# Kernel optimization log

Measured on AMD Instinct MI355X. Metric: run time of the kernel, lower is better.

Reference implementation:

```python
import jax, jax.numpy as jnp
import numpy as np

B, C, H, W, K = 4, 96, 56, 56, 9
CM = 2 * C  # graph-conv output channels (standard Grapher: 2*in_channels)


def setup_inputs() -> dict:
    key = jax.random.key(0)
    ks = jax.random.split(key, 6)
    x = jax.random.normal(ks[0], (B, C, H, W), jnp.float32)
    fc1_w = jax.random.normal(ks[1], (C, C), jnp.float32) * 0.05
    fc1_b = jnp.zeros((C,), jnp.float32)
    gconv_w = jax.random.normal(ks[2], (CM, 2 * C), jnp.float32) * 0.05
    gconv_b = jnp.zeros((CM,), jnp.float32)
    fc2_w = jax.random.normal(ks[3], (C, CM), jnp.float32) * 0.05
    fc2_b = jnp.zeros((C,), jnp.float32)
    sa_w = jax.random.normal(ks[4], (1, 2, 7, 7), jnp.float32) * 0.05
    return dict(x=x, fc1_w=fc1_w, fc1_b=fc1_b, gconv_w=gconv_w, gconv_b=gconv_b,
                fc2_w=fc2_w, fc2_b=fc2_b, sa_w=sa_w)


def _knn_idx(xf, k):
    # xf: (B, C, N) -> (B, N, k) nearest-neighbor indices (includes self),
    # matching dense_knn_matrix: topk of negative squared euclidean distance.
    x2 = jnp.sum(xf * xf, axis=1)                       # (B, N)
    inner = jnp.einsum('bcn,bcm->bnm', xf, xf)          # (B, N, N)
    dist = x2[:, :, None] - 2.0 * inner + x2[:, None, :]
    _, idx = jax.lax.top_k(-dist, k)                    # (B, N, k)
    return idx


def _grapher(x, fc1_w, fc1_b, gconv_w, gconv_b, fc2_w, fc2_b, sa_w):
    shortcut = x
    # fc1: 1x1 conv C -> C
    h = jnp.einsum('bchw,oc->bohw', x, fc1_w) + fc1_b[None, :, None, None]
    b, c, hh, ww = h.shape
    n = hh * ww
    xf = h.reshape(b, c, n)                              # nodes: (B, C, N)
    idx = _knn_idx(xf, K)                                # dynamic KNN graph
    # EdgeConv2d: gather x_j at neighbor indices, x_i = center
    xt = jnp.transpose(xf, (0, 2, 1))                    # (B, N, C)
    x_j = jax.vmap(lambda t, i: t[i])(xt, idx)           # (B, N, K, C)
    x_j = jnp.transpose(x_j, (0, 3, 1, 2))               # (B, C, N, K)
    x_i = xf[:, :, :, None]                              # (B, C, N, 1)
    feat = jnp.concatenate(
        [jnp.broadcast_to(x_i, x_j.shape), x_j - x_i], axis=1)  # (B, 2C, N, K)
    e = jnp.einsum('bcnk,oc->bonk', feat, gconv_w) + gconv_b[None, :, None, None]
    e = jax.nn.relu(e)
    g = jnp.max(e, axis=-1)                              # max over K neighbors
    g = g.reshape(b, CM, hh, ww)
    # fc2: 1x1 conv 2C -> C
    out = jnp.einsum('bchw,oc->bohw', g, fc2_w) + fc2_b[None, :, None, None]
    # SpatialAttention: channel mean/max -> 7x7 conv -> sigmoid gate
    avg = jnp.mean(out, axis=1, keepdims=True)
    mx = jnp.max(out, axis=1, keepdims=True)
    sa_in = jnp.concatenate([avg, mx], axis=1)           # (B, 2, H, W)
    att = jax.lax.conv_general_dilated(
        sa_in, sa_w, window_strides=(1, 1), padding=[(3, 3), (3, 3)],
        dimension_numbers=('NCHW', 'OIHW', 'NCHW'))
    att = jax.nn.sigmoid(att)
    return out * att + shortcut


def reference(x, fc1_w, fc1_b, gconv_w, gconv_b, fc2_w, fc2_b, sa_w):
    return _grapher(x, fc1_w, fc1_b, gconv_w, gconv_b, fc2_w, fc2_b, sa_w)
```

## Files before the change

### kernel.cpp

```cpp
#include <hip/hip_runtime.h>

#define BB 4
#define CC 96
#define NN 3136
#define FLTMAX 3.402823466e+38f
#define CAP 44
#define DELTA 1.0f
#define PREF_MARGIN 0.8f

typedef unsigned short ushort_t;
typedef __attribute__((ext_vector_type(8))) short bf16x8;
typedef __attribute__((ext_vector_type(4))) float f32x4;

__device__ __forceinline__ ushort_t f2bf(float f) {
    unsigned u = __float_as_uint(f);
    unsigned r = (u + 0x7fff + ((u >> 16) & 1)) >> 16;
    return (ushort_t)r;
}
__device__ __forceinline__ float bf2f(ushort_t us) {
    return __uint_as_float(((unsigned)us) << 16);
}


__global__ __launch_bounds__(256) void k_fc1(const float* __restrict__ x, const float* __restrict__ w,
                                             const float* __restrict__ bias, float* __restrict__ h,
                                             float* __restrict__ x2g,
                                             ushort_t* __restrict__ hAhi,
                                             float* __restrict__ hT) {
    __shared__ float sm[96 * 98 + 96 * 64];
    float* wT = sm;
    float* xl = sm + 96 * 98;
    const int tid = threadIdx.x;
    const int n0 = blockIdx.x * 64;
    const int b = blockIdx.y;
    for (int i = tid; i < 96 * 96; i += 256) {
        int o = i / 96, c = i - o * 96;
        wT[c * 98 + o] = w[i];
    }
    const float* xb = x + (size_t)b * CC * NN;
    for (int i = tid; i < 96 * 64; i += 256) {
        int c = i >> 6, nl = i & 63;
        xl[i] = xb[(size_t)c * NN + n0 + nl];
    }
    __syncthreads();
    const int tr = tid >> 4, tc = tid & 15;
    float acc[6][4];
#pragma unroll
    for (int i = 0; i < 6; ++i)
#pragma unroll
        for (int j = 0; j < 4; ++j) acc[i][j] = 0.f;
#pragma unroll 4
    for (int c = 0; c < 96; ++c) {
        float4 xv = *(const float4*)&xl[c * 64 + tc * 4];
        const float* wp = &wT[c * 98 + tr * 6];
        float2 w01 = *(const float2*)(wp);
        float2 w23 = *(const float2*)(wp + 2);
        float2 w45 = *(const float2*)(wp + 4);
        float wv[6] = {w01.x, w01.y, w23.x, w23.y, w45.x, w45.y};
        float xj[4] = {xv.x, xv.y, xv.z, xv.w};
#pragma unroll
        for (int i = 0; i < 6; ++i)
#pragma unroll
            for (int j = 0; j < 4; ++j) acc[i][j] = fmaf(wv[i], xj[j], acc[i][j]);
    }
    float* hb = h + (size_t)b * CC * NN;
    float* hTb = hT + (size_t)b * NN * 96;
    ushort_t* thi = hAhi + (size_t)b * 602112;
#pragma unroll
    for (int i = 0; i < 6; ++i) {
        float bi = bias[tr * 6 + i];
        acc[i][0] += bi; acc[i][1] += bi; acc[i][2] += bi; acc[i][3] += bi;
        float4 o4 = make_float4(acc[i][0], acc[i][1], acc[i][2], acc[i][3]);
        *(float4*)&hb[(size_t)(tr * 6 + i) * NN + n0 + tc * 4] = o4;
        const int c = tr * 6 + i;
        const int cpart = c >> 3;
#pragma unroll
        for (int j = 0; j < 4; ++j) {
            const int n = n0 + tc * 4 + j;
            const int idx = (((n >> 5) * 12 + cpart) * 32 + (n & 31)) * 8 + (c & 7);
            thi[idx] = f2bf(acc[i][j]);
            hTb[(size_t)n * 96 + c] = acc[i][j];
        }
    }
    __syncthreads();
#pragma unroll
    for (int j = 0; j < 4; ++j) {
        float s = 0.f;
#pragma unroll
        for (int i = 0; i < 6; ++i) s = fmaf(acc[i][j], acc[i][j], s);
        sm[tr * 64 + tc * 4 + j] = s;
    }
    __syncthreads();
    if (tid < 64) {
        float s = 0.f;
#pragma unroll
        for (int t = 0; t < 16; ++t) s += sm[t * 64 + tid];
        x2g[(size_t)b * NN + n0 + tid] = s;
    }
}

#define MFMA_TILE_HI(t, acc0, acc1, acc2, acc3)                                       \
    {                                                                                 \
        const int abase_ = (t) * 6144;                                                \
        _Pragma("unroll")                                                             \
        for (int ks_ = 0; ks_ < 3; ++ks_) {                                           \
            const int base_ = abase_ + ks_ * 1024;                                    \
            bf16x8 a0_ = *(const bf16x8*)(hHi + base_ + aoff0);                       \
            bf16x8 a1_ = *(const bf16x8*)(hHi + base_ + aoff1);                       \
            bf16x8 a2_ = *(const bf16x8*)(hHi + base_ + 3072 + aoff0);                \
            bf16x8 a3_ = *(const bf16x8*)(hHi + base_ + 3072 + aoff1);                \
            acc0 = __builtin_amdgcn_mfma_f32_16x16x32_bf16(a0_, bhi[ks_], acc0, 0, 0, 0); \
            acc1 = __builtin_amdgcn_mfma_f32_16x16x32_bf16(a1_, bhi[ks_], acc1, 0, 0, 0); \
            acc2 = __builtin_amdgcn_mfma_f32_16x16x32_bf16(a2_, bhi[ks_], acc2, 0, 0, 0); \
            acc3 = __builtin_amdgcn_mfma_f32_16x16x32_bf16(a3_, bhi[ks_], acc3, 0, 0, 0); \
        }                                                                             \
    }

__global__ __launch_bounds__(256) void k_dist(const ushort_t* __restrict__ hAhi,
                                              const float* __restrict__ x2,
                                              int* __restrict__ cand_cnt,
                                              int* __restrict__ cand_idx) {
    __shared__ float thrb[32][24];
    __shared__ float thr_s[32];
    __shared__ int   cnt[32];
    __shared__ int   list[32][CAP];
    const int tid = threadIdx.x;
    const int nb = blockIdx.x, q = blockIdx.y, b = blockIdx.z;
    const int w = tid >> 6, l = tid & 63;
    const int ln = l & 15, lq = l >> 4;
    const int p = w >> 1;
    const int kl_off = lq * 256;
    const ushort_t* hHi = hAhi + (size_t)b * 602112;
    const float* x2b = x2 + (size_t)b * NN;

    const int lane32n = (w & 1) * 16 + ln;
    bf16x8 bhi[3];
#pragma unroll
    for (int ks = 0; ks < 3; ++ks) {
        const int off = nb * 3072 + ks * 1024 + kl_off + lane32n * 8;
        bhi[ks] = *(const bf16x8*)(hHi + off);
    }
    const int aoff0 = kl_off + ln * 8;
    const int aoff1 = kl_off + (16 + ln) * 8;

    const int qb0 = (q == 0) ? 0 : (q == 1) ? 13 : (q == 2) ? 25 : 37;
    const int qb1 = (q == 0) ? 13 : (q == 1) ? 25 : (q == 2) ? 37 : 49;
    const int tstart = qb0 + p;

    unsigned scache[7][8];
    float lv0 = FLTMAX, lv1 = FLTMAX, lv2 = FLTMAX;
#pragma unroll
    for (int ti = 0; ti < 7; ++ti) {
        const int t = tstart + 2 * ti;
        if (t < qb1) {
            const int m0 = t * 64;
            f32x4 acc0 = {0.f, 0.f, 0.f, 0.f}, acc1 = {0.f, 0.f, 0.f, 0.f};
            f32x4 acc2 = {0.f, 0.f, 0.f, 0.f}, acc3 = {0.f, 0.f, 0.f, 0.f};
            MFMA_TILE_HI(t, acc0, acc1, acc2, acc3);
#pragma unroll
            for (int msub = 0; msub < 4; ++msub) {
                f32x4 a = (msub == 0) ? acc0 : (msub == 1) ? acc1 : (msub == 2) ? acc2 : acc3;
                const int mb = m0 + msub * 16 + lq * 4;
                float4 xv = *(const float4*)&x2b[mb];
                float s0 = fmaf(-2.f, a[0], xv.x);
                float s1 = fmaf(-2.f, a[1], xv.y);
                float s2 = fmaf(-2.f, a[2], xv.z);
                float s3 = fmaf(-2.f, a[3], xv.w);
                scache[ti][msub * 2 + 0] = ((unsigned)f2bf(s0) << 16) | (unsigned)f2bf(s1);
                scache[ti][msub * 2 + 1] = ((unsigned)f2bf(s2) << 16) | (unsigned)f2bf(s3);
                float ss[4] = {s0, s1, s2, s3};
#pragma unroll
                for (int r = 0; r < 4; ++r) {
                    float v = ss[r];
                    float t0 = fminf(lv0, v);
                    lv0 = fmaxf(t0, lv1);
                    float t1 = fminf(t0, lv1);
                    lv1 = fmaxf(t1, lv2);
                    lv2 = fminf(t1, lv2);
                }
            }
        }
    }
    {
        const int sidx = (p * 4 + lq) * 3;
        thrb[lane32n][sidx + 0] = lv0;
        thrb[lane32n][sidx + 1] = lv1;
        thrb[lane32n][sidx + 2] = lv2;
    }
    __syncthreads();
    if (tid < 32) {
        float tmp[24];
#pragma unroll
        for (int j = 0; j < 24; ++j) tmp[j] = thrb[tid][j];
        float last = FLTMAX;
        for (int kk = 0; kk < 9; ++kk) {
            float mn = FLTMAX; int ms = 0;
            for (int j = 0; j < 24; ++j)
                if (tmp[j] < mn) { mn = tmp[j]; ms = j; }
            tmp[ms] = FLTMAX;
            last = mn;
        }
        thr_s[tid] = last + DELTA;
        cnt[tid] = 0;
    }
    __syncthreads();
    const float thr = thr_s[lane32n];

#pragma unroll
    for (int ti = 0; ti < 7; ++ti) {
        const int t = tstart + 2 * ti;
        if (t < qb1) {
            const int m0 = t * 64;
#pragma unroll
            for (int msub = 0; msub < 4; ++msub) {
                const int mb = m0 + msub * 16 + lq * 4;
                const unsigned u01 = scache[ti][msub * 2 + 0];
                const unsigned u23 = scache[ti][msub * 2 + 1];
                unsigned bits[4] = {u01 >> 16, u01 & 0xffffu, u23 >> 16, u23 & 0xffffu};
#pragma unroll
                for (int r = 0; r < 4; ++r) {
                    if (bf2f((ushort_t)bits[r]) <= thr) {
                        int pos = atomicAdd(&cnt[lane32n], 1);
                        if (pos < CAP) list[lane32n][pos] = (int)((bits[r] << 16) | (unsigned)(mb + r));
                    }
                }
            }
        }
    }
    __syncthreads();
    const size_t rowbase = (size_t)b * NN + nb * 32;
    if (tid < 32) cand_cnt[(rowbase + tid) * 4 + q] = min(cnt[tid], CAP);
    for (int i = tid; i < 32 * CAP; i += 256) {
        int r = i / CAP, j = i - r * CAP;
        if (j < min(cnt[r], CAP))
            cand_idx[((rowbase + r) * 4 + q) * CAP + j] = list[r][j];
    }
}

__global__ __launch_bounds__(256) void k_merge9(const int* __restrict__ cand_cnt,
                                                const int* __restrict__ cand_idx,
                                                const float* __restrict__ hT,
                                                const float* __restrict__ x2,
                                                int* __restrict__ idx9) {
    const int tid = threadIdx.x;
    const int wv = tid >> 6, lane = tid & 63;
    const size_t n = (size_t)blockIdx.x * 4 + wv;
    const int b = (int)(n / NN);
    const int nn = (int)(n - (size_t)b * NN);
    const int c0 = cand_cnt[n * 4 + 0];
    const int c1 = cand_cnt[n * 4 + 1];
    const int c2 = cand_cnt[n * 4 + 2];
    const int c3 = cand_cnt[n * 4 + 3];
    const int p1 = c0, p2 = c0 + c1, p3 = c0 + c1 + c2;
    const int ct = p3 + c3;
    const float* hTb = hT + (size_t)b * NN * 96;
    const float* own = hTb + (size_t)nn * 96;
    const float* x2b = x2 + (size_t)b * NN;

    float av[3]; int cjs[3];
#pragma unroll
    for (int t = 0; t < 3; ++t) { av[t] = FLTMAX; cjs[t] = 0x7fffffff; }
#pragma unroll
    for (int t = 0; t < 3; ++t) {
        const int j = lane + 64 * t;
        if (j < ct) {
            const int qq = (j >= p1) + (j >= p2) + (j >= p3);
            const int base = (qq == 0) ? 0 : (qq == 1) ? p1 : (qq == 2) ? p2 : p3;
            const unsigned u = (unsigned)cand_idx[(n * 4 + qq) * CAP + (j - base)];
            av[t] = bf2f((ushort_t)(u >> 16));
            cjs[t] = (int)(u & 0xffffu);
        }
    }
    float a9 = FLTMAX;
    {
        float tv[3] = {av[0], av[1], av[2]};
        for (int kk = 0; kk < 9; ++kk) {
            float mv = tv[0]; int ms = 0;
            if (tv[1] < mv) { mv = tv[1]; ms = 1; }
            if (tv[2] < mv) { mv = tv[2]; ms = 2; }
            int mid = lane * 4 + ms;
#pragma unroll
            for (int s = 32; s; s >>= 1) {
                float ov = __shfl_xor(mv, s, 64);
                int oi = __shfl_xor(mid, s, 64);
                if (ov < mv || (ov == mv && oi < mid)) { mv = ov; mid = oi; }
            }
            a9 = mv;
            if ((mid >> 2) == lane) tv[mid & 3] = FLTMAX;
        }
    }
    const float cutoff = a9 + PREF_MARGIN;

    float vs[3];
#pragma unroll
    for (int t = 0; t < 3; ++t) {
        vs[t] = FLTMAX;
        if (av[t] <= cutoff) {
            const int cj = cjs[t];
            const float* cr = hTb + (size_t)cj * 96;
            float dot = 0.f;
#pragma unroll
            for (int i = 0; i < 24; ++i) {
                float4 rv = *(const float4*)&own[i * 4];
                float4 cv4 = *(const float4*)&cr[i * 4];
                dot = fmaf(rv.x, cv4.x, dot);
                dot = fmaf(rv.y, cv4.y, dot);
                dot = fmaf(rv.z, cv4.z, dot);
                dot = fmaf(rv.w, cv4.w, dot);
            }
            vs[t] = fmaf(-2.f, dot, x2b[cj]);
        }
    }
    int* dst = idx9 + n * 9;
    for (int kk = 0; kk < 9; ++kk) {
        float mv = vs[0]; int mi = cjs[0];
        if (vs[1] < mv || (vs[1] == mv && cjs[1] < mi)) { mv = vs[1]; mi = cjs[1]; }
        if (vs[2] < mv || (vs[2] == mv && cjs[2] < mi)) { mv = vs[2]; mi = cjs[2]; }
#pragma unroll
        for (int s = 32; s; s >>= 1) {
            float ov = __shfl_xor(mv, s, 64);
            int oi = __shfl_xor(mi, s, 64);
            if (ov < mv || (ov == mv && oi < mi)) { mv = ov; mi = oi; }
        }
        if (lane == 0) dst[kk] = mi;
#pragma unroll
        for (int t = 0; t < 3; ++t)
            if (cjs[t] == mi) vs[t] = FLTMAX;
    }
}

__global__ __launch_bounds__(256) void k_ac(const float* __restrict__ h, const float* __restrict__ gw,
                                            const float* __restrict__ gb, ushort_t* __restrict__ acT) {
    __shared__ float sm[96 * 98 + 96 * 64];
    float* wT = sm;
    float* hl = sm + 96 * 98;
    const int tid = threadIdx.x;
    const int n0 = blockIdx.x * 64, ot = blockIdx.y, b = blockIdx.z;
    for (int i = tid; i < 96 * 96; i += 256) {
        int o = i / 96, c = i - o * 96;
        float v;
        if (ot < 2) {
            const float* gwp = gw + (size_t)(ot * 96 + o) * 192;
            v = gwp[c] - gwp[96 + c];
        } else {
            v = gw[(size_t)((ot - 2) * 96 + o) * 192 + 96 + c];
        }
        wT[c * 98 + o] = v;
    }
    const float* hb = h + (size_t)b * CC * NN;
    for (int i = tid; i < 96 * 64; i += 256) {
        int c = i >> 6, nl = i & 63;
        hl[i] = hb[(size_t)c * NN + n0 + nl];
    }
    __syncthreads();
    const int tr = tid >> 4, tc = tid & 15;
    float acc[6][4];
#pragma unroll
    for (int i = 0; i < 6; ++i)
#pragma unroll
        for (int j = 0; j < 4; ++j) acc[i][j] = 0.f;
#pragma unroll 4
    for (int c = 0; c < 96; ++c) {
        float4 xv = *(const float4*)&hl[c * 64 + tc * 4];
        const float* wp = &wT[c * 98 + tr * 6];
        float2 w01 = *(const float2*)(wp);
        float2 w23 = *(const float2*)(wp + 2);
        float2 w45 = *(const float2*)(wp + 4);
        float wv[6] = {w01.x, w01.y, w23.x, w23.y, w45.x, w45.y};
        float xj[4] = {xv.x, xv.y, xv.z, xv.w};
#pragma unroll
        for (int i = 0; i < 6; ++i)
#pragma unroll
            for (int j = 0; j < 4; ++j) acc[i][j] = fmaf(wv[i], xj[j], acc[i][j]);
    }
    const int obase = ot * 96 + tr * 6;
    float bs[6];
#pragma unroll
    for (int i = 0; i < 6; ++i) bs[i] = (ot < 2) ? gb[obase + i] : 0.f;
#pragma unroll
    for (int j = 0; j < 4; ++j) {
        ushort_t* dst = acT + ((size_t)b * NN + n0 + tc * 4 + j) * 384 + obase;
        ushort2 p0, p1, p2;
        p0.x = f2bf(acc[0][j] + bs[0]); p0.y = f2bf(acc[1][j] + bs[1]);
        p1.x = f2bf(acc[2][j] + bs[2]); p1.y = f2bf(acc[3][j] + bs[3]);
        p2.x = f2bf(acc[4][j] + bs[4]); p2.y = f2bf(acc[5][j] + bs[5]);
        *(ushort2*)(dst + 0) = p0;
        *(ushort2*)(dst + 2) = p1;
        *(ushort2*)(dst + 4) = p2;
    }
}

__global__ __launch_bounds__(256) void k_gather(const ushort_t* __restrict__ acT,
                                                const int* __restrict__ idx9,
                                                float* __restrict__ gT) {
    const int lane = threadIdx.x & 63;
    const int wv = threadIdx.x >> 6;
    const int b = blockIdx.y;
    const int nb = blockIdx.x * 16 + wv * 4;
    for (int r = 0; r < 4; ++r) {
        const int n = nb + r;
        const ushort_t* ar = acT + ((size_t)b * NN + n) * 384;
        float a0 = bf2f(ar[lane]), a1 = bf2f(ar[lane + 64]), a2 = bf2f(ar[lane + 128]);
        const int* ip = idx9 + ((size_t)b * NN + n) * 9;
        int jj[9];
#pragma unroll
        for (int k = 0; k < 9; ++k) jj[k] = ip[k];
        float m0 = -FLTMAX, m1 = -FLTMAX, m2 = -FLTMAX;
#pragma unroll
        for (int k = 0; k < 9; ++k) {
            const ushort_t* cr = acT + ((size_t)b * NN + jj[k]) * 384 + 192;
            m0 = fmaxf(m0, a0 + bf2f(cr[lane]));
            m1 = fmaxf(m1, a1 + bf2f(cr[lane + 64]));
            m2 = fmaxf(m2, a2 + bf2f(cr[lane + 128]));
        }
        float* gr = gT + ((size_t)b * NN + n) * 192;
        gr[lane] = fmaxf(m0, 0.f);
        gr[lane + 64] = fmaxf(m1, 0.f);
        gr[lane + 128] = fmaxf(m2, 0.f);
    }
}

__global__ __launch_bounds__(256) void k_fc2(const float* __restrict__ gT, const float* __restrict__ w,
                                             const float* __restrict__ bias, float* __restrict__ out,
                                             float* __restrict__ sa_in) {
    __shared__ float Wc[96 * 36];
    __shared__ float Gc[16 * 36];
    __shared__ float red[2][16][17];
    const int tid = threadIdx.x;
    const int n0 = blockIdx.x * 16, b = blockIdx.y;
    const int tr = tid >> 4, tc = tid & 15;
    float acc[6];
#pragma unroll
    for (int i = 0; i < 6; ++i) acc[i] = 0.f;
    for (int kc = 0; kc < 192; kc += 32) {
        for (int i = tid; i < 96 * 32; i += 256) {
            int c = i >> 5, k = i & 31;
            Wc[c * 36 + k] = w[(size_t)c * 192 + kc + k];
        }
        for (int i = tid; i < 16 * 32; i += 256) {
            int nl = i >> 5, k = i & 31;
            Gc[nl * 36 + k] = gT[((size_t)b * NN + n0 + nl) * 192 + kc + k];
        }
        __syncthreads();
#pragma unroll
        for (int k = 0; k < 32; k += 4) {
            float4 gv = *(const float4*)&Gc[tc * 36 + k];
#pragma unroll
            for (int i = 0; i < 6; ++i) {
                float4 wv = *(const float4*)&Wc[(tr * 6 + i) * 36 + k];
                acc[i] = fmaf(wv.x, gv.x, acc[i]);
                acc[i] = fmaf(wv.y, gv.y, acc[i]);
                acc[i] = fmaf(wv.z, gv.z, acc[i]);
                acc[i] = fmaf(wv.w, gv.w, acc[i]);
            }
        }
        __syncthreads();
    }
    float* ob = out + (size_t)b * CC * NN;
    float ps = 0.f, pm = -FLTMAX;
#pragma unroll
    for (int i = 0; i < 6; ++i) {
        float o = acc[i] + bias[tr * 6 + i];
        ob[(size_t)(tr * 6 + i) * NN + n0 + tc] = o;
        ps += o;
        pm = fmaxf(pm, o);
    }
    red[0][tr][tc] = ps;
    red[1][tr][tc] = pm;
    __syncthreads();
    if (tid < 16) {
        float s_ = 0.f, m_ = -FLTMAX;
#pragma unroll
        for (int t = 0; t < 16; ++t) { s_ += red[0][t][tid]; m_ = fmaxf(m_, red[1][t][tid]); }
        sa_in[(size_t)b * 2 * NN + n0 + tid] = s_ * (1.0f / 96.0f);
        sa_in[(size_t)b * 2 * NN + NN + n0 + tid] = m_;
    }
}

__global__ __launch_bounds__(256) void k_att(const float* __restrict__ sa_in, const float* __restrict__ sw,
                                             const float* __restrict__ x, float* __restrict__ out) {
    int n = blockIdx.x * 256 + threadIdx.x;
    int b = blockIdx.y;
    if (n >= NN) return;
    int y = n / 56, xw = n - y * 56;
    float acc = 0.f;
#pragma unroll
    for (int ci = 0; ci < 2; ++ci) {
        const float* sb = sa_in + ((size_t)b * 2 + ci) * NN;
#pragma unroll
        for (int dy = 0; dy < 7; ++dy) {
            int yy = y + dy - 3;
            if ((unsigned)yy < 56u) {
#pragma unroll
                for (int dx = 0; dx < 7; ++dx) {
                    int xx = xw + dx - 3;
                    if ((unsigned)xx < 56u)
                        acc = fmaf(sb[yy * 56 + xx], sw[(ci * 7 + dy) * 7 + dx], acc);
                }
            }
        }
    }
    float att = 1.f / (1.f + expf(-acc));
    const float* xb = x + (size_t)b * CC * NN + n;
    float* ob = out + (size_t)b * CC * NN + n;
#pragma unroll 4
    for (int c = 0; c < 96; ++c) {
        size_t o = (size_t)c * NN;
        ob[o] = fmaf(ob[o], att, xb[o]);
    }
}

extern "C" void kernel_launch(void* const* d_in, const int* in_sizes, int n_in,
                              void* d_out, int out_size, void* d_ws, size_t ws_size,
                              hipStream_t stream) {
    (void)in_sizes; (void)n_in; (void)out_size; (void)ws_size;
    const float* x       = (const float*)d_in[0];
    const float* fc1_w   = (const float*)d_in[1];
    const float* fc1_b   = (const float*)d_in[2];
    const float* gconv_w = (const float*)d_in[3];
    const float* gconv_b = (const float*)d_in[4];
    const float* fc2_w   = (const float*)d_in[5];
    const float* fc2_b   = (const float*)d_in[6];
    const float* sa_w    = (const float*)d_in[7];
    float* out = (float*)d_out;

    float* ws   = (float*)d_ws;
    float* h    = ws;
    float* x2   = h + (size_t)BB * CC * NN;
    int*   idx9 = (int*)(x2 + BB * NN);
    float* regA = (float*)(idx9 + (size_t)BB * NN * 9);
    ushort_t* hAhi = (ushort_t*)regA;
    ushort_t* acT  = (ushort_t*)regA;
    float* hT   = regA + 2408448;
    float* regB = hT + 1204224;
    int*   cand_idx = (int*)regB;
    int*   cand_cnt = (int*)(regB + 2207744);
    float* gT   = regB;
    float* sa_in = regB + 2408448;

    k_fc1   <<<dim3(49, BB), 256, 0, stream>>>(x, fc1_w, fc1_b, h, x2, hAhi, hT);
    k_dist  <<<dim3(98, 4, BB), 256, 0, stream>>>(hAhi, x2, cand_cnt, cand_idx);
    k_merge9<<<dim3(3136), 256, 0, stream>>>(cand_cnt, cand_idx, hT, x2, idx9);
    k_ac    <<<dim3(49, 4, BB), 256, 0, stream>>>(h, gconv_w, gconv_b, acT);
    k_gather<<<dim3(196, BB), 256, 0, stream>>>(acT, idx9, gT);
    k_fc2   <<<dim3(196, BB), 256, 0, stream>>>(gT, fc2_w, fc2_b, out, sa_in);
    k_att   <<<dim3(13, BB), 256, 0, stream>>>(sa_in, sa_w, x, out);
}
```

Baseline: 250.7 us.

## Replace merge9 iterative top-9 with threshold cutoff and rank-based selection

k_dist now writes each row's per-quarter threshold to global memory. k_merge9 uses the smallest of the four thresholds as its cutoff instead of running a 9-round wave-reduction top-9 over the approximate bf16 distances. Surviving candidates get exact fp32 distances and are appended to a shared-memory list. Each entry's rank is then counted by all-pairs comparison, and entries with rank below 9 are written directly, replacing the second 9-round shuffle reduction. Cutting those serialized shuffle reductions should shorten merge9. The cutoff is looser than the old a9+0.8, so more exact dot products may be computed, and the all-pairs ranking is quadratic in the number of survivors.

```diff
diff --git a/kernel.cpp b/kernel.cpp
--- a/kernel.cpp
+++ b/kernel.cpp
@@ -6,7 +6,6 @@
 #define FLTMAX 3.402823466e+38f
 #define CAP 44
 #define DELTA 1.0f
-#define PREF_MARGIN 0.8f
 
 typedef unsigned short ushort_t;
 typedef __attribute__((ext_vector_type(8))) short bf16x8;
@@ -119,7 +118,8 @@
 __global__ __launch_bounds__(256) void k_dist(const ushort_t* __restrict__ hAhi,
                                               const float* __restrict__ x2,
                                               int* __restrict__ cand_cnt,
-                                              int* __restrict__ cand_idx) {
+                                              int* __restrict__ cand_idx,
+                                              float* __restrict__ thr_row) {
     __shared__ float thrb[32][24];
     __shared__ float thr_s[32];
     __shared__ int   cnt[32];
@@ -202,6 +202,7 @@
         }
         thr_s[tid] = last + DELTA;
         cnt[tid] = 0;
+        thr_row[((size_t)b * NN + nb * 32 + tid) * 4 + q] = last + DELTA;
     }
     __syncthreads();
     const float thr = thr_s[lane32n];
@@ -239,9 +240,12 @@
 
 __global__ __launch_bounds__(256) void k_merge9(const int* __restrict__ cand_cnt,
                                                 const int* __restrict__ cand_idx,
+                                                const float* __restrict__ thr_row,
                                                 const float* __restrict__ hT,
                                                 const float* __restrict__ x2,
                                                 int* __restrict__ idx9) {
+    __shared__ int  np[4];
+    __shared__ int2 pl[4][192];
     const int tid = threadIdx.x;
     const int wv = tid >> 6, lane = tid & 63;
     const size_t n = (size_t)blockIdx.x * 4 + wv;
@@ -253,13 +257,12 @@
     const int c3 = cand_cnt[n * 4 + 3];
     const int p1 = c0, p2 = c0 + c1, p3 = c0 + c1 + c2;
     const int ct = p3 + c3;
+    const float cutoff = fminf(fminf(thr_row[n * 4 + 0], thr_row[n * 4 + 1]),
+                               fminf(thr_row[n * 4 + 2], thr_row[n * 4 + 3]));
+    if (lane == 0) np[wv] = 0;
     const float* hTb = hT + (size_t)b * NN * 96;
     const float* own = hTb + (size_t)nn * 96;
     const float* x2b = x2 + (size_t)b * NN;
-
-    float av[3]; int cjs[3];
-#pragma unroll
-    for (int t = 0; t < 3; ++t) { av[t] = FLTMAX; cjs[t] = 0x7fffffff; }
 #pragma unroll
     for (int t = 0; t < 3; ++t) {
         const int j = lane + 64 * t;
@@ -267,65 +270,48 @@
             const int qq = (j >= p1) + (j >= p2) + (j >= p3);
             const int base = (qq == 0) ? 0 : (qq == 1) ? p1 : (qq == 2) ? p2 : p3;
             const unsigned u = (unsigned)cand_idx[(n * 4 + qq) * CAP + (j - base)];
-            av[t] = bf2f((ushort_t)(u >> 16));
-            cjs[t] = (int)(u & 0xffffu);
-        }
-    }
-    float a9 = FLTMAX;
-    {
-        float tv[3] = {av[0], av[1], av[2]};
-        for (int kk = 0; kk < 9; ++kk) {
-            float mv = tv[0]; int ms = 0;
-            if (tv[1] < mv) { mv = tv[1]; ms = 1; }
-            if (tv[2] < mv) { mv = tv[2]; ms = 2; }
-            int mid = lane * 4 + ms;
-#pragma unroll
-            for (int s = 32; s; s >>= 1) {
-                float ov = __shfl_xor(mv, s, 64);
-                int oi = __shfl_xor(mid, s, 64);
-                if (ov < mv || (ov == mv && oi < mid)) { mv = ov; mid = oi; }
+            const float av = bf2f((ushort_t)(u >> 16));
+            if (av <= cutoff) {
+                const int cj = (int)(u & 0xffffu);
+                const float* cr = hTb + (size_t)cj * 96;
+                float dot = 0.f;
+#pragma unroll
+                for (int i = 0; i < 24; ++i) {
+                    float4 rv = *(const float4*)&own[i * 4];
+                    float4 cv4 = *(const float4*)&cr[i * 4];
+                    dot = fmaf(rv.x, cv4.x, dot);
+                    dot = fmaf(rv.y, cv4.y, dot);
+                    dot = fmaf(rv.z, cv4.z, dot);
+                    dot = fmaf(rv.w, cv4.w, dot);
+                }
+                const float v = fmaf(-2.f, dot, x2b[cj]);
+                const int pos = atomicAdd(&np[wv], 1);
+                pl[wv][pos] = make_int2(__float_as_int(v), cj);
             }
-            a9 = mv;
-            if ((mid >> 2) == lane) tv[mid & 3] = FLTMAX;
-        }
-    }
-    const float cutoff = a9 + PREF_MARGIN;
-
-    float vs[3];
+        }
+    }
+    const int npw = np[wv];
+    int2 mine[3]; int rk[3];
 #pragma unroll
     for (int t = 0; t < 3; ++t) {
-        vs[t] = FLTMAX;
-        if (av[t] <= cutoff) {
-            const int cj = cjs[t];
-            const float* cr = hTb + (size_t)cj * 96;
-            float dot = 0.f;
-#pragma unroll
-            for (int i = 0; i < 24; ++i) {
-                float4 rv = *(const float4*)&own[i * 4];
-                float4 cv4 = *(const float4*)&cr[i * 4];
-                dot = fmaf(rv.x, cv4.x, dot);
-                dot = fmaf(rv.y, cv4.y, dot);
-                dot = fmaf(rv.z, cv4.z, dot);
-                dot = fmaf(rv.w, cv4.w, dot);
-            }
-            vs[t] = fmaf(-2.f, dot, x2b[cj]);
+        const int s = lane + 64 * t;
+        mine[t] = (s < npw) ? pl[wv][s] : make_int2(0x7f7fffff, 0x7fffffff);
+        rk[t] = 0;
+    }
+    for (int j2 = 0; j2 < npw; ++j2) {
+        const int2 e = pl[wv][j2];
+        const float ev = __int_as_float(e.x);
+#pragma unroll
+        for (int t = 0; t < 3; ++t) {
+            const float mv = __int_as_float(mine[t].x);
+            rk[t] += (ev < mv || (ev == mv && e.y < mine[t].y)) ? 1 : 0;
         }
     }
     int* dst = idx9 + n * 9;
-    for (int kk = 0; kk < 9; ++kk) {
-        float mv = vs[0]; int mi = cjs[0];
-        if (vs[1] < mv || (vs[1] == mv && cjs[1] < mi)) { mv = vs[1]; mi = cjs[1]; }
-        if (vs[2] < mv || (vs[2] == mv && cjs[2] < mi)) { mv = vs[2]; mi = cjs[2]; }
-#pragma unroll
-        for (int s = 32; s; s >>= 1) {
-            float ov = __shfl_xor(mv, s, 64);
-            int oi = __shfl_xor(mi, s, 64);
-            if (ov < mv || (ov == mv && oi < mi)) { mv = ov; mi = oi; }
-        }
-        if (lane == 0) dst[kk] = mi;
-#pragma unroll
-        for (int t = 0; t < 3; ++t)
-            if (cjs[t] == mi) vs[t] = FLTMAX;
+#pragma unroll
+    for (int t = 0; t < 3; ++t) {
+        const int s = lane + 64 * t;
+        if (s < npw && rk[t] < 9) dst[rk[t]] = mine[t].y;
     }
 }
 
@@ -535,12 +521,13 @@
     float* regB = hT + 1204224;
     int*   cand_idx = (int*)regB;
     int*   cand_cnt = (int*)(regB + 2207744);
+    float* thr_row  = regB + 2207744 + 50176;
     float* gT   = regB;
     float* sa_in = regB + 2408448;
 
     k_fc1   <<<dim3(49, BB), 256, 0, stream>>>(x, fc1_w, fc1_b, h, x2, hAhi, hT);
-    k_dist  <<<dim3(98, 4, BB), 256, 0, stream>>>(hAhi, x2, cand_cnt, cand_idx);
-    k_merge9<<<dim3(3136), 256, 0, stream>>>(cand_cnt, cand_idx, hT, x2, idx9);
+    k_dist  <<<dim3(98, 4, BB), 256, 0, stream>>>(hAhi, x2, cand_cnt, cand_idx, thr_row);
+    k_merge9<<<dim3(3136), 256, 0, stream>>>(cand_cnt, cand_idx, thr_row, hT, x2, idx9);
     k_ac    <<<dim3(49, 4, BB), 256, 0, stream>>>(h, gconv_w, gconv_b, acT);
     k_gather<<<dim3(196, BB), 256, 0, stream>>>(acT, idx9, gT);
     k_fc2   <<<dim3(196, BB), 256, 0, stream>>>(gT, fc2_w, fc2_b, out, sa_in);
```

Result: no change. 248.2 us (-1.0%).
